# Kernel optimization log

Hardware: AMD Instinct MI355X
Metric: run time of the kernel (lower is better)

Reference implementation:

```python
import jax, jax.numpy as jnp
import numpy as np

BN_EPS = 1e-5


def _gcn(x, A, W, gamma, beta):
    # x: [B,N,Cin], A: [B,N,N] -> [B,N,Cout]; BatchNorm1d over (B,N) per channel (train-mode batch stats)
    h = jnp.einsum('bnm,bmc->bnc', A, x @ W)
    mu = h.mean(axis=(0, 1))
    var = h.var(axis=(0, 1))
    h = (h - mu) * jax.lax.rsqrt(var + BN_EPS) * gamma + beta
    return jax.nn.relu(h)  # dropout is identity (drop_prob=0 / eval)


def _ppige(x, A, W0, g0, b0, W_res, g_res, b_res):
    h = _gcn(x, A, W0, g0, b0)
    for i in range(W_res.shape[0]):  # residual GCN stack (num_GCN-1 layers)
        h = _gcn(h, A, W_res[i], g_res[i], b_res[i]) + h
    return h


def _gge(x, w1, b1, w2, b2):
    return jax.nn.relu(jax.nn.relu(x @ w1 + b1) @ w2 + b2)


def _gaga(G, h):
    # G: [B,N,H], h: [B,H]
    att = jax.nn.softmax(jnp.einsum('bnh,bh->bn', G, h), axis=-1)
    return jnp.einsum('bnh,bn->bh', G, att)


def _led(ea, eb, conv_w, conv_b, p1_w, p1_b, p2_w, p2_b):
    # ea, eb: [B, 2H]; Conv1d(2H->2H, k=1) over length-2 axis then MaxPool1d(2)
    stacked = jnp.stack([ea, eb], axis=-1)  # [B, 2H, 2]
    conv = jnp.einsum('oc,bct->bot', conv_w, stacked) + conv_b[None, :, None]
    cnn_x = conv.max(axis=-1)  # [B, 2H]
    x = jax.nn.relu(jnp.concatenate([cnn_x, ea - eb], axis=1) @ p1_w + p1_b)
    return x @ p2_w + p2_b


def setup_inputs() -> dict:
    key = jax.random.key(0)
    ks = jax.random.split(key, 24)
    Bs, N, PPI_in, H, F_in = 8, 2048, 512, 256, 1024
    n_res = 3  # num_GCN - 1
    s = 0.02
    adjA = jax.random.uniform(ks[0], (Bs, N, N), jnp.float32)
    adjB = jax.random.uniform(ks[1], (Bs, N, N), jnp.float32)
    adjA = adjA / adjA.sum(-1, keepdims=True)  # row-normalized for numerical sanity
    adjB = adjB / adjB.sum(-1, keepdims=True)
    return {
        'a': jax.random.normal(ks[2], (Bs, F_in), jnp.float32),
        'bio_a': jax.random.normal(ks[3], (Bs, N, PPI_in), jnp.float32),
        'A': adjA,
        'b': jax.random.normal(ks[4], (Bs, F_in), jnp.float32),
        'bio_b': jax.random.normal(ks[5], (Bs, N, PPI_in), jnp.float32),
        'B': adjB,
        'W0': jax.random.normal(ks[6], (PPI_in, H), jnp.float32) * s,
        'gamma0': jnp.ones((H,), jnp.float32),
        'beta0': jnp.zeros((H,), jnp.float32),
        'W_res': jax.random.normal(ks[7], (n_res, H, H), jnp.float32) * s,
        'gamma_res': jnp.ones((n_res, H), jnp.float32),
        'beta_res': jnp.zeros((n_res, H), jnp.float32),
        'g1_w': jax.random.normal(ks[8], (F_in, 128), jnp.float32) * s,
        'g1_b': jnp.zeros((128,), jnp.float32),
        'g2_w': jax.random.normal(ks[9], (128, H), jnp.float32) * s,
        'g2_b': jnp.zeros((H,), jnp.float32),
        'conv_w': jax.random.normal(ks[10], (2 * H, 2 * H), jnp.float32) * s,
        'conv_b': jnp.zeros((2 * H,), jnp.float32),
        'p1_w': jax.random.normal(ks[11], (4 * H, H), jnp.float32) * s,
        'p1_b': jnp.zeros((H,), jnp.float32),
        'p2_w': jax.random.normal(ks[12], (H, 2), jnp.float32) * s,
        'p2_b': jnp.zeros((2,), jnp.float32),
    }


def reference(a, bio_a, A, b, bio_b, B, W0, gamma0, beta0, W_res, gamma_res, beta_res,
              g1_w, g1_b, g2_w, g2_b, conv_w, conv_b, p1_w, p1_b, p2_w, p2_b):
    Ga = _ppige(bio_a, A, W0, gamma0, beta0, W_res, gamma_res, beta_res)
    Gb = _ppige(bio_b, B, W0, gamma0, beta0, W_res, gamma_res, beta_res)
    ha = _gge(a, g1_w, g1_b, g2_w, g2_b)
    hb = _gge(b, g1_w, g1_b, g2_w, g2_b)
    ea = jnp.concatenate([ha, _gaga(Ga, ha)], axis=-1)
    eb = jnp.concatenate([hb, _gaga(Gb, hb)], axis=-1)
    logits = _led(ea, eb, conv_w, conv_b, p1_w, p1_b, p2_w, p2_b)
    return jax.nn.log_softmax(logits, axis=-1)
```

## Files before the change

kernel.cpp:

```cpp
#include <hip/hip_runtime.h>
#include <hip/hip_bf16.h>
#include <cstdint>

typedef unsigned short u16;
typedef __bf16 bf16x8 __attribute__((ext_vector_type(8)));
typedef float f32x4 __attribute__((ext_vector_type(4)));

typedef __attribute__((address_space(1))) const void* gas_ptr;
typedef __attribute__((address_space(3))) void* las_ptr;

__device__ __forceinline__ u16 f2bf(float f) {
  union { __hip_bfloat16 h; u16 u; } v;
  v.h = __float2bfloat16(f);
  return v.u;
}
__device__ __forceinline__ float bf2f(u16 u) {
  union { unsigned int i; float f; } v;
  v.i = ((unsigned int)u) << 16;
  return v.f;
}

__device__ __forceinline__ void gload16(const u16* g, u16* l) {
  __builtin_amdgcn_global_load_lds((gas_ptr)g, (las_ptr)l, 16, 0, 0);
}

__global__ __launch_bounds__(256) void k_convert_all(const float* __restrict__ aA,
                                                     const float* __restrict__ aB,
                                                     const float* __restrict__ bA,
                                                     const float* __restrict__ bB,
                                                     u16* __restrict__ Abf,
                                                     u16* __restrict__ biobf) {
  long e0 = ((long)blockIdx.x * 256 + threadIdx.x) * 16;
  const float* src; u16* dst;
  if (e0 < 33554432L)        { src = aA;              dst = Abf; }
  else if (e0 < 67108864L)   { src = aB - 33554432L;  dst = Abf; }
  else if (e0 < 75497472L)   { src = bA - 67108864L;  dst = biobf - 67108864L; }
  else                       { src = bB - 75497472L;  dst = biobf - 75497472L + 8388608L; }
  float4 v0 = *reinterpret_cast<const float4*>(src + e0);
  float4 v1 = *reinterpret_cast<const float4*>(src + e0 + 4);
  float4 v2 = *reinterpret_cast<const float4*>(src + e0 + 8);
  float4 v3 = *reinterpret_cast<const float4*>(src + e0 + 12);
  union { u16 u[8]; uint4 q; } o0, o1;
  o0.u[0] = f2bf(v0.x); o0.u[1] = f2bf(v0.y); o0.u[2] = f2bf(v0.z); o0.u[3] = f2bf(v0.w);
  o0.u[4] = f2bf(v1.x); o0.u[5] = f2bf(v1.y); o0.u[6] = f2bf(v1.z); o0.u[7] = f2bf(v1.w);
  o1.u[0] = f2bf(v2.x); o1.u[1] = f2bf(v2.y); o1.u[2] = f2bf(v2.z); o1.u[3] = f2bf(v2.w);
  o1.u[4] = f2bf(v3.x); o1.u[5] = f2bf(v3.y); o1.u[6] = f2bf(v3.z); o1.u[7] = f2bf(v3.w);
  *reinterpret_cast<uint4*>(dst + e0) = o0.q;
  *reinterpret_cast<uint4*>(dst + e0 + 8) = o1.q;
}

__global__ __launch_bounds__(256) void k_prep_weights(const float* __restrict__ W0,
                                                      const float* __restrict__ Wres,
                                                      u16* __restrict__ W0t,
                                                      u16* __restrict__ Wrt) {
  __shared__ float tile[32][33];
  int y = blockIdx.y;
  const float* src; u16* dst; int R, r0;
  if (y < 16) { src = W0; dst = W0t; R = 512; r0 = y * 32; }
  else {
    int i = (y - 16) >> 3;
    src = Wres + i * 65536; dst = Wrt + i * 65536; R = 256; r0 = ((y - 16) & 7) * 32;
  }
  const int C = 256;
  int c0 = blockIdx.x * 32;
  int tx = threadIdx.x & 31, ty = threadIdx.x >> 5;
#pragma unroll
  for (int i = 0; i < 4; ++i) {
    int r = ty + i * 8;
    tile[r][tx] = src[(long)(r0 + r) * C + c0 + tx];
  }
  __syncthreads();
#pragma unroll
  for (int i = 0; i < 4; ++i) {
    int c = ty + i * 8;
    dst[(long)(c0 + c) * R + r0 + tx] = f2bf(tile[tx][c]);
  }
}

template<int EPI, int SWZ>
__global__ __launch_bounds__(256) void k_gemm(const u16* __restrict__ A, int lda, long sA,
                                              const u16* __restrict__ Bt, int ldb, long sB,
                                              u16* __restrict__ C, int ldc, long sC,
                                              u16* __restrict__ PtOut, int ldpt,
                                              float* __restrict__ stats, int K) {
  __shared__ __align__(16) u16 smem[4][8192];
  __shared__ float cs[256];
  const int tid = threadIdx.x;
  const int lane = tid & 63;
  const int wid = tid >> 6;
  const int wm = wid >> 1, wn = wid & 1;

  int bx = blockIdx.x, by = blockIdx.y, bz = blockIdx.z;
  if (SWZ) {
    int lin = bx + 16 * by + 32 * bz;
    int swz = (lin & 7) * 64 + (lin >> 3);
    bx = swz & 15; by = (swz >> 4) & 1; bz = swz >> 5;
  }
  const long m0 = (long)bx * 128, n0 = (long)by * 128;
  const int z = bz;
  const u16* Ab = A + (long)z * sA;
  const u16* Btb = Bt + (long)z * sB;

  const int rsub = lane >> 3;
  const int swzcol = ((lane & 7) ^ rsub) * 8;
  const long a_row = m0 + wid * 32 + rsub;
  const long b_row = n0 + wid * 32 + rsub;

  if (EPI == 0) cs[tid] = 0.f;

  const f32x4 zero = {0.f, 0.f, 0.f, 0.f};
  f32x4 acc[4][4];
#pragma unroll
  for (int i = 0; i < 4; ++i)
#pragma unroll
    for (int j = 0; j < 4; ++j) acc[i][j] = zero;

  const int fr = lane & 15;
  const int kgrp = lane >> 4;
  const int swz_rd = lane & 7;
  const int nk = K >> 6;

  auto stage = [&](int buf, int k0) {
#pragma unroll
    for (int i = 0; i < 4; ++i)
      gload16(Ab + (a_row + i * 8) * lda + (k0 + swzcol), &smem[buf][(wid * 32 + i * 8) * 64]);
#pragma unroll
    for (int i = 0; i < 4; ++i)
      gload16(Btb + (b_row + i * 8) * ldb + (k0 + swzcol), &smem[2 + buf][(wid * 32 + i * 8) * 64]);
  };

  stage(0, 0);
  __syncthreads();
  for (int t = 0; t < nk; ++t) {
    int cur = t & 1;
    if (t + 1 < nk) stage(1 - cur, (t + 1) * 64);
    const u16* Asb = smem[cur];
    const u16* Bsb = smem[2 + cur];
#pragma unroll
    for (int ks = 0; ks < 2; ++ks) {
      bf16x8 af[4], bfv[4];
#pragma unroll
      for (int f = 0; f < 4; ++f) {
        int cA = (ks * 4 + kgrp) ^ swz_rd;
        af[f]  = *reinterpret_cast<const bf16x8*>(&Asb[(wm * 64 + f * 16 + fr) * 64 + cA * 8]);
        bfv[f] = *reinterpret_cast<const bf16x8*>(&Bsb[(wn * 64 + f * 16 + fr) * 64 + cA * 8]);
      }
#pragma unroll
      for (int mf = 0; mf < 4; ++mf)
#pragma unroll
        for (int nf = 0; nf < 4; ++nf)
          acc[mf][nf] = __builtin_amdgcn_mfma_f32_16x16x32_bf16(af[mf], bfv[nf], acc[mf][nf], 0, 0, 0);
    }
    __syncthreads();
  }

  if (EPI == 0) {
    u16* Cb = C + (long)z * sC;
    const int side = z >> 3;
#pragma unroll
    for (int mf = 0; mf < 4; ++mf) {
      long mrow = m0 + wm * 64 + mf * 16 + kgrp * 4;
#pragma unroll
      for (int nf = 0; nf < 4; ++nf) {
        long ncol = n0 + wn * 64 + nf * 16 + fr;
#pragma unroll
        for (int r = 0; r < 4; ++r)
          Cb[(mrow + r) * ldc + ncol] = f2bf(acc[mf][nf][r]);
      }
    }
#pragma unroll
    for (int nf = 0; nf < 4; ++nf) {
      int cl = wn * 64 + nf * 16 + fr;
      float s = 0.f, q = 0.f;
#pragma unroll
      for (int mf = 0; mf < 4; ++mf)
#pragma unroll
        for (int r = 0; r < 4; ++r) { float v = acc[mf][nf][r]; s += v; q += v * v; }
      atomicAdd(&cs[cl], s);
      atomicAdd(&cs[128 + cl], q);
    }
    __syncthreads();
    if (tid < 128) atomicAdd(&stats[side * 512 + n0 + tid], cs[tid]);
    else           atomicAdd(&stats[side * 512 + 256 + n0 + (tid - 128)], cs[tid]);
  } else {
    u16* Ts = &smem[0][0];
#pragma unroll
    for (int mf = 0; mf < 4; ++mf)
#pragma unroll
      for (int nf = 0; nf < 4; ++nf) {
        int nl = wn * 64 + nf * 16 + fr;
        int ml = wm * 64 + mf * 16 + kgrp * 4;
#pragma unroll
        for (int r = 0; r < 4; ++r)
          Ts[nl * 136 + ml + r] = f2bf(acc[mf][nf][r]);
      }
    __syncthreads();
    int n = tid >> 1, half = tid & 1;
    const u16* sp = Ts + n * 136 + half * 64;
    u16* dp = PtOut + (long)(n0 + n) * ldpt + m0 + half * 64;
#pragma unroll
    for (int j = 0; j < 8; ++j)
      reinterpret_cast<uint4*>(dp)[j] = reinterpret_cast<const uint4*>(sp)[j];
  }
}

__global__ __launch_bounds__(256) void k_bn_apply(const ushort4* __restrict__ u4,
                                                  ushort4* __restrict__ h4,
                                                  const float* __restrict__ statsL,
                                                  const float* __restrict__ gamma,
                                                  const float* __restrict__ beta, int res) {
  long i = (long)blockIdx.x * 256 + threadIdx.x;
  int side = (int)(i >> 20);
  int c0 = (int)(i & 63) * 4;
  const float* st = statsL + side * 512;
  ushort4 uv = u4[i];
  float vp[4] = { bf2f(uv.x), bf2f(uv.y), bf2f(uv.z), bf2f(uv.w) };
  float rp[4];
#pragma unroll
  for (int j = 0; j < 4; ++j) {
    int c = c0 + j;
    float mu = st[c] * (1.f / 16384.f);
    float var = st[256 + c] * (1.f / 16384.f) - mu * mu;
    float sc = gamma[c] * rsqrtf(var + 1e-5f);
    float sh = beta[c] - mu * sc;
    rp[j] = fmaxf(vp[j] * sc + sh, 0.f);
  }
  if (res) {
    ushort4 hv = h4[i];
    rp[0] += bf2f(hv.x); rp[1] += bf2f(hv.y); rp[2] += bf2f(hv.z); rp[3] += bf2f(hv.w);
  }
  ushort4 o;
  o.x = f2bf(rp[0]); o.y = f2bf(rp[1]); o.z = f2bf(rp[2]); o.w = f2bf(rp[3]);
  h4[i] = o;
}

__global__ __launch_bounds__(256) void k_gge(const float* __restrict__ in_a,
                                             const float* __restrict__ in_b,
                                             const float* __restrict__ w1, const float* __restrict__ b1,
                                             const float* __restrict__ w2, const float* __restrict__ b2,
                                             float* __restrict__ ha) {
  __shared__ float av[1024];
  __shared__ float hid[128];
  int bx = blockIdx.x, t = threadIdx.x;
  const float* ap = ((bx >> 3) ? in_b : in_a) + (bx & 7) * 1024;
  for (int i = t; i < 1024; i += 256) av[i] = ap[i];
  __syncthreads();
  if (t < 128) {
    float s = b1[t];
    for (int c = 0; c < 1024; ++c) s += av[c] * w1[c * 128 + t];
    hid[t] = fmaxf(s, 0.f);
  }
  __syncthreads();
  float s = b2[t];
  for (int c = 0; c < 128; ++c) s += hid[c] * w2[c * 256 + t];
  ha[bx * 256 + t] = fmaxf(s, 0.f);
}

__global__ __launch_bounds__(256) void k_gaga_scores(const u16* __restrict__ h,
                                                     const float* __restrict__ ha,
                                                     float* __restrict__ sc) {
  __shared__ __align__(16) float has[256];
  int bx = blockIdx.x;
  has[threadIdx.x] = ha[bx * 256 + threadIdx.x];
  __syncthreads();
  const u16* G = h + (long)bx * 524288;
  int wv = threadIdx.x >> 6, lane = threadIdx.x & 63;
  float4 h4 = reinterpret_cast<const float4*>(has)[lane];
  for (int i = 0; i < 32; ++i) {
    int n = blockIdx.y * 128 + wv * 32 + i;
    ushort4 v = reinterpret_cast<const ushort4*>(G + (long)n * 256)[lane];
    float d = bf2f(v.x) * h4.x + bf2f(v.y) * h4.y + bf2f(v.z) * h4.z + bf2f(v.w) * h4.w;
#pragma unroll
    for (int o2 = 32; o2 > 0; o2 >>= 1) d += __shfl_down(d, o2);
    if (lane == 0) sc[bx * 2048 + n] = d;
  }
}

__global__ __launch_bounds__(256) void k_softmax2048(const float* __restrict__ sc, float* __restrict__ att) {
  __shared__ float red[256];
  int b = blockIdx.x, t = threadIdx.x;
  const float* s = sc + b * 2048;
  float* o = att + b * 2048;
  float v[8];
  float m = -1e30f;
#pragma unroll
  for (int i = 0; i < 8; ++i) { v[i] = s[t + i * 256]; m = fmaxf(m, v[i]); }
  red[t] = m; __syncthreads();
  for (int o2 = 128; o2 > 0; o2 >>= 1) { if (t < o2) red[t] = fmaxf(red[t], red[t + o2]); __syncthreads(); }
  m = red[0]; __syncthreads();
  float sum = 0.f;
#pragma unroll
  for (int i = 0; i < 8; ++i) { v[i] = expf(v[i] - m); sum += v[i]; }
  red[t] = sum; __syncthreads();
  for (int o2 = 128; o2 > 0; o2 >>= 1) { if (t < o2) red[t] += red[t + o2]; __syncthreads(); }
  float inv = 1.f / red[0];
#pragma unroll
  for (int i = 0; i < 8; ++i) o[t + i * 256] = v[i] * inv;
}

__global__ __launch_bounds__(256) void k_gaga_out(const u16* __restrict__ h,
                                                  const float* __restrict__ att,
                                                  float* __restrict__ ga) {
  __shared__ float atts[128];
  int bx = blockIdx.x, n0 = blockIdx.y * 128, c = threadIdx.x;
  if (threadIdx.x < 128) atts[threadIdx.x] = att[bx * 2048 + n0 + threadIdx.x];
  __syncthreads();
  const u16* base = h + (long)bx * 524288 + (long)n0 * 256 + c;
  float s = 0.f;
#pragma unroll 4
  for (int i = 0; i < 128; ++i) s += bf2f(base[(long)i * 256]) * atts[i];
  atomicAdd(&ga[bx * 256 + c], s);
}

__global__ __launch_bounds__(512) void k_led_conv(const float* __restrict__ ha, const float* __restrict__ ga,
                                                  const float* __restrict__ hb, const float* __restrict__ gb,
                                                  const float* __restrict__ cw, const float* __restrict__ cb,
                                                  float* __restrict__ cnn, float* __restrict__ diff) {
  __shared__ float ea[8][512], eb[8][512];
  int t = threadIdx.x;
  for (int i = t; i < 4096; i += 512) {
    int b = i >> 9, c = i & 511;
    float va = (c < 256) ? ha[b * 256 + c] : ga[b * 256 + c - 256];
    float vb = (c < 256) ? hb[b * 256 + c] : gb[b * 256 + c - 256];
    ea[b][c] = va; eb[b][c] = vb;
    if (blockIdx.x == 0) diff[i] = va - vb;
  }
  __syncthreads();
  int o = blockIdx.x * 64 + (t >> 3), b = t & 7;
  const float* wr = cw + (long)o * 512;
  float s0 = cb[o], s1 = s0;
  for (int c = 0; c < 512; ++c) { float w = wr[c]; s0 += w * ea[b][c]; s1 += w * eb[b][c]; }
  cnn[b * 512 + o] = fmaxf(s0, s1);
}

__global__ __launch_bounds__(256) void k_led_p1(const float* __restrict__ cnn, const float* __restrict__ diff,
                                                const float* __restrict__ w, const float* __restrict__ pb,
                                                float* __restrict__ x) {
  __shared__ float cat[8][1024];
  int t = threadIdx.x;
  for (int i = t; i < 8192; i += 256) {
    int b = i >> 10, c = i & 1023;
    cat[b][c] = (c < 512) ? cnn[b * 512 + c] : diff[b * 512 + c - 512];
  }
  __syncthreads();
  int o = blockIdx.x * 32 + (t >> 3), b = t & 7;
  float s = pb[o];
  for (int c = 0; c < 1024; ++c) s += cat[b][c] * w[c * 256 + o];
  x[b * 256 + o] = fmaxf(s, 0.f);
}

__global__ __launch_bounds__(64) void k_led_final(const float* __restrict__ x,
                                                  const float* __restrict__ p2w, const float* __restrict__ p2b,
                                                  float* __restrict__ out) {
  __shared__ float lg[16];
  int t = threadIdx.x;
  if (t < 16) {
    int b = t >> 1, j = t & 1;
    float s = p2b[j];
    for (int c = 0; c < 256; ++c) s += x[b * 256 + c] * p2w[c * 2 + j];
    lg[t] = s;
  }
  __syncthreads();
  if (t < 8) {
    float l0 = lg[t * 2], l1 = lg[t * 2 + 1];
    float m = fmaxf(l0, l1);
    float lse = m + logf(expf(l0 - m) + expf(l1 - m));
    out[t * 2] = l0 - lse;
    out[t * 2 + 1] = l1 - lse;
  }
}

extern "C" void kernel_launch(void* const* d_in, const int* in_sizes, int n_in,
                              void* d_out, int out_size, void* d_ws, size_t ws_size,
                              hipStream_t stream) {
  const float* in_a   = (const float*)d_in[0];
  const float* bio_a  = (const float*)d_in[1];
  const float* adj_a  = (const float*)d_in[2];
  const float* in_b   = (const float*)d_in[3];
  const float* bio_b  = (const float*)d_in[4];
  const float* adj_b  = (const float*)d_in[5];
  const float* W0     = (const float*)d_in[6];
  const float* gamma0 = (const float*)d_in[7];
  const float* beta0  = (const float*)d_in[8];
  const float* W_res  = (const float*)d_in[9];
  const float* g_res  = (const float*)d_in[10];
  const float* b_res  = (const float*)d_in[11];
  const float* g1_w   = (const float*)d_in[12];
  const float* g1_b   = (const float*)d_in[13];
  const float* g2_w   = (const float*)d_in[14];
  const float* g2_b   = (const float*)d_in[15];
  const float* conv_w = (const float*)d_in[16];
  const float* conv_b = (const float*)d_in[17];
  const float* p1_w   = (const float*)d_in[18];
  const float* p1_b   = (const float*)d_in[19];
  const float* p2_w   = (const float*)d_in[20];
  const float* p2_b   = (const float*)d_in[21];
  float* out = (float*)d_out;

  char* ws = (char*)d_ws;
  size_t off = 0;
  auto alloc = [&](size_t bytes) {
    char* p = ws + off;
    off += (bytes + 255) & ~(size_t)255;
    return p;
  };
  u16*   Abf   = (u16*)  alloc(67108864ull * 2);
  u16*   biobf = (u16*)  alloc(16777216ull * 2);
  u16*   Pt    = (u16*)  alloc(8388608ull * 2);
  u16*   ubf   = (u16*)  alloc(8388608ull * 2);
  u16*   hbf   = (u16*)  alloc(8388608ull * 2);
  u16*   W0t   = (u16*)  alloc(131072ull * 2);
  u16*   Wrt   = (u16*)  alloc(196608ull * 2);
  float* stats = (float*)alloc(4096 * 4);
  float* gabuf = (float*)alloc(4096 * 4);
  float* hav   = (float*)alloc(4096 * 4);
  float* scb   = (float*)alloc(32768 * 4);
  float* attb  = (float*)alloc(32768 * 4);
  float* cnn   = (float*)alloc(4096 * 4);
  float* diff  = (float*)alloc(4096 * 4);
  float* xbuf  = (float*)alloc(2048 * 4);

  k_prep_weights<<<dim3(8, 40), 256, 0, stream>>>(W0, W_res, W0t, Wrt);
  (void)hipMemsetAsync(stats, 0, 32768, stream);

  k_convert_all<<<20480, 256, 0, stream>>>(adj_a, adj_b, bio_a, bio_b, Abf, biobf);

  for (int layer = 0; layer < 4; ++layer) {
    const u16* Ain = (layer == 0) ? biobf : hbf;
    int K = (layer == 0) ? 512 : 256;
    const u16* Wt = (layer == 0) ? W0t : (Wrt + (layer - 1) * 65536);
    float* statsL = stats + layer * 1024;
    const float* gm = (layer == 0) ? gamma0 : (g_res + (layer - 1) * 256);
    const float* bt = (layer == 0) ? beta0 : (b_res + (layer - 1) * 256);

    k_gemm<1, 0><<<dim3(256, 2, 1), 256, 0, stream>>>(Ain, K, 0, Wt, K, 0,
                                                      nullptr, 0, 0, Pt, 32768, nullptr, K);
    k_gemm<0, 1><<<dim3(16, 2, 16), 256, 0, stream>>>(Abf, 2048, 4194304L, Pt, 32768, 2048,
                                                      ubf, 256, 524288L, nullptr, 0, statsL, 2048);
    k_bn_apply<<<8192, 256, 0, stream>>>((const ushort4*)ubf, (ushort4*)hbf,
                                         statsL, gm, bt, layer ? 1 : 0);
  }

  k_gge<<<16, 256, 0, stream>>>(in_a, in_b, g1_w, g1_b, g2_w, g2_b, hav);
  k_gaga_scores<<<dim3(16, 16), 256, 0, stream>>>(hbf, hav, scb);
  k_softmax2048<<<16, 256, 0, stream>>>(scb, attb);
  k_gaga_out<<<dim3(16, 16), 256, 0, stream>>>(hbf, attb, gabuf);

  k_led_conv<<<8, 512, 0, stream>>>(hav, gabuf, hav + 2048, gabuf + 2048, conv_w, conv_b, cnn, diff);
  k_led_p1<<<8, 256, 0, stream>>>(cnn, diff, p1_w, p1_b, xbuf);
  k_led_final<<<1, 64, 0, stream>>>(xbuf, p2_w, p2_b, out);
}
```

Baseline: 555.1 us.

## Fuse fp32-to-bf16 conversion into first-layer GEMMs and drop standalone convert pass

```diff
diff --git a/kernel.cpp b/kernel.cpp
--- a/kernel.cpp
+++ b/kernel.cpp
@@ -22,31 +22,6 @@
 
 __device__ __forceinline__ void gload16(const u16* g, u16* l) {
   __builtin_amdgcn_global_load_lds((gas_ptr)g, (las_ptr)l, 16, 0, 0);
-}
-
-__global__ __launch_bounds__(256) void k_convert_all(const float* __restrict__ aA,
-                                                     const float* __restrict__ aB,
-                                                     const float* __restrict__ bA,
-                                                     const float* __restrict__ bB,
-                                                     u16* __restrict__ Abf,
-                                                     u16* __restrict__ biobf) {
-  long e0 = ((long)blockIdx.x * 256 + threadIdx.x) * 16;
-  const float* src; u16* dst;
-  if (e0 < 33554432L)        { src = aA;              dst = Abf; }
-  else if (e0 < 67108864L)   { src = aB - 33554432L;  dst = Abf; }
-  else if (e0 < 75497472L)   { src = bA - 67108864L;  dst = biobf - 67108864L; }
-  else                       { src = bB - 75497472L;  dst = biobf - 75497472L + 8388608L; }
-  float4 v0 = *reinterpret_cast<const float4*>(src + e0);
-  float4 v1 = *reinterpret_cast<const float4*>(src + e0 + 4);
-  float4 v2 = *reinterpret_cast<const float4*>(src + e0 + 8);
-  float4 v3 = *reinterpret_cast<const float4*>(src + e0 + 12);
-  union { u16 u[8]; uint4 q; } o0, o1;
-  o0.u[0] = f2bf(v0.x); o0.u[1] = f2bf(v0.y); o0.u[2] = f2bf(v0.z); o0.u[3] = f2bf(v0.w);
-  o0.u[4] = f2bf(v1.x); o0.u[5] = f2bf(v1.y); o0.u[6] = f2bf(v1.z); o0.u[7] = f2bf(v1.w);
-  o1.u[0] = f2bf(v2.x); o1.u[1] = f2bf(v2.y); o1.u[2] = f2bf(v2.z); o1.u[3] = f2bf(v2.w);
-  o1.u[4] = f2bf(v3.x); o1.u[5] = f2bf(v3.y); o1.u[6] = f2bf(v3.z); o1.u[7] = f2bf(v3.w);
-  *reinterpret_cast<uint4*>(dst + e0) = o0.q;
-  *reinterpret_cast<uint4*>(dst + e0 + 8) = o1.q;
 }
 
 __global__ __launch_bounds__(256) void k_prep_weights(const float* __restrict__ W0,
@@ -77,12 +52,15 @@
   }
 }
 
-template<int EPI, int SWZ>
-__global__ __launch_bounds__(256) void k_gemm(const u16* __restrict__ A, int lda, long sA,
-                                              const u16* __restrict__ Bt, int ldb, long sB,
-                                              u16* __restrict__ C, int ldc, long sC,
-                                              u16* __restrict__ PtOut, int ldpt,
-                                              float* __restrict__ stats, int K) {
+template<int EPI, int SWZ, int CVT>
+__global__ __launch_bounds__(256) void k_gemm(
+    const u16* __restrict__ A, int lda, long sA,
+    const float* __restrict__ Afa, const float* __restrict__ Afb,
+    long splitRow, int ldaf, long zrows, u16* __restrict__ AbfOut,
+    const u16* __restrict__ Bt, int ldb, long sB,
+    u16* __restrict__ C, int ldc, long sC,
+    u16* __restrict__ PtOut, int ldpt,
+    float* __restrict__ stats, int K) {
   __shared__ __align__(16) u16 smem[4][8192];
   __shared__ float cs[256];
   const int tid = threadIdx.x;
@@ -91,10 +69,12 @@
   const int wm = wid >> 1, wn = wid & 1;
 
   int bx = blockIdx.x, by = blockIdx.y, bz = blockIdx.z;
-  if (SWZ) {
+  if (SWZ == 1) {
     int lin = bx + 16 * by + 32 * bz;
     int swz = (lin & 7) * 64 + (lin >> 3);
     bx = swz & 15; by = (swz >> 4) & 1; bz = swz >> 5;
+  } else if (SWZ == 2) {
+    int t = bx; bx = by; by = t;
   }
   const long m0 = (long)bx * 128, n0 = (long)by * 128;
   const int z = bz;
@@ -120,22 +100,17 @@
   const int swz_rd = lane & 7;
   const int nk = K >> 6;
 
-  auto stage = [&](int buf, int k0) {
+  auto stageA = [&](int buf, int k0) {
 #pragma unroll
     for (int i = 0; i < 4; ++i)
       gload16(Ab + (a_row + i * 8) * lda + (k0 + swzcol), &smem[buf][(wid * 32 + i * 8) * 64]);
+  };
+  auto stageB = [&](int buf, int k0) {
 #pragma unroll
     for (int i = 0; i < 4; ++i)
       gload16(Btb + (b_row + i * 8) * ldb + (k0 + swzcol), &smem[2 + buf][(wid * 32 + i * 8) * 64]);
   };
-
-  stage(0, 0);
-  __syncthreads();
-  for (int t = 0; t < nk; ++t) {
-    int cur = t & 1;
-    if (t + 1 < nk) stage(1 - cur, (t + 1) * 64);
-    const u16* Asb = smem[cur];
-    const u16* Bsb = smem[2 + cur];
+  auto compute = [&](const u16* Asb, const u16* Bsb) {
 #pragma unroll
     for (int ks = 0; ks < 2; ++ks) {
       bf16x8 af[4], bfv[4];
@@ -151,8 +126,61 @@
         for (int nf = 0; nf < 4; ++nf)
           acc[mf][nf] = __builtin_amdgcn_mfma_f32_16x16x32_bf16(af[mf], bfv[nf], acc[mf][nf], 0, 0, 0);
     }
+  };
+
+#define RLOADA(k0)                                                                       \
+  {                                                                                      \
+    _Pragma("unroll")                                                                    \
+    for (int i = 0; i < 4; ++i) {                                                        \
+      long R = (long)z * zrows + a_row + i * 8;                                          \
+      const float* sp = (R < splitRow ? Afa + R * (long)ldaf                             \
+                                      : Afb + (R - splitRow) * (long)ldaf) + (k0) + swzcol; \
+      rg[i * 2]     = *reinterpret_cast<const float4*>(sp);                              \
+      rg[i * 2 + 1] = *reinterpret_cast<const float4*>(sp + 4);                          \
+    }                                                                                    \
+  }
+#define CVTWRITEA(buf, k0)                                                               \
+  {                                                                                      \
+    _Pragma("unroll")                                                                    \
+    for (int i = 0; i < 4; ++i) {                                                        \
+      union { u16 u[8]; uint4 q; } o;                                                    \
+      o.u[0] = f2bf(rg[i*2].x);   o.u[1] = f2bf(rg[i*2].y);                              \
+      o.u[2] = f2bf(rg[i*2].z);   o.u[3] = f2bf(rg[i*2].w);                              \
+      o.u[4] = f2bf(rg[i*2+1].x); o.u[5] = f2bf(rg[i*2+1].y);                            \
+      o.u[6] = f2bf(rg[i*2+1].z); o.u[7] = f2bf(rg[i*2+1].w);                            \
+      *reinterpret_cast<uint4*>(&smem[buf][(wid * 32 + i * 8) * 64 + lane * 8]) = o.q;   \
+      if (AbfOut && by == 0) {                                                           \
+        long R = (long)z * zrows + a_row + i * 8;                                        \
+        *reinterpret_cast<uint4*>(AbfOut + R * (long)ldaf + (k0) + swzcol) = o.q;        \
+      }                                                                                  \
+    }                                                                                    \
+  }
+
+  if constexpr (CVT) {
+    float4 rg[8];
+    RLOADA(0);
+    stageB(0, 0);
+    CVTWRITEA(0, 0);
     __syncthreads();
-  }
+    for (int t = 0; t < nk; ++t) {
+      int cur = t & 1;
+      if (t + 1 < nk) { RLOADA((t + 1) * 64); stageB(1 - cur, (t + 1) * 64); }
+      compute(smem[cur], smem[2 + cur]);
+      if (t + 1 < nk) CVTWRITEA(1 - cur, (t + 1) * 64);
+      __syncthreads();
+    }
+  } else {
+    stageA(0, 0); stageB(0, 0);
+    __syncthreads();
+    for (int t = 0; t < nk; ++t) {
+      int cur = t & 1;
+      if (t + 1 < nk) { stageA(1 - cur, (t + 1) * 64); stageB(1 - cur, (t + 1) * 64); }
+      compute(smem[cur], smem[2 + cur]);
+      __syncthreads();
+    }
+  }
+#undef RLOADA
+#undef CVTWRITEA
 
   if (EPI == 0) {
     u16* Cb = C + (long)z * sC;
@@ -405,7 +433,6 @@
     return p;
   };
   u16*   Abf   = (u16*)  alloc(67108864ull * 2);
-  u16*   biobf = (u16*)  alloc(16777216ull * 2);
   u16*   Pt    = (u16*)  alloc(8388608ull * 2);
   u16*   ubf   = (u16*)  alloc(8388608ull * 2);
   u16*   hbf   = (u16*)  alloc(8388608ull * 2);
@@ -423,20 +450,27 @@
   k_prep_weights<<<dim3(8, 40), 256, 0, stream>>>(W0, W_res, W0t, Wrt);
   (void)hipMemsetAsync(stats, 0, 32768, stream);
 
-  k_convert_all<<<20480, 256, 0, stream>>>(adj_a, adj_b, bio_a, bio_b, Abf, biobf);
-
   for (int layer = 0; layer < 4; ++layer) {
-    const u16* Ain = (layer == 0) ? biobf : hbf;
-    int K = (layer == 0) ? 512 : 256;
-    const u16* Wt = (layer == 0) ? W0t : (Wrt + (layer - 1) * 65536);
     float* statsL = stats + layer * 1024;
     const float* gm = (layer == 0) ? gamma0 : (g_res + (layer - 1) * 256);
     const float* bt = (layer == 0) ? beta0 : (b_res + (layer - 1) * 256);
 
-    k_gemm<1, 0><<<dim3(256, 2, 1), 256, 0, stream>>>(Ain, K, 0, Wt, K, 0,
-                                                      nullptr, 0, 0, Pt, 32768, nullptr, K);
-    k_gemm<0, 1><<<dim3(16, 2, 16), 256, 0, stream>>>(Abf, 2048, 4194304L, Pt, 32768, 2048,
-                                                      ubf, 256, 524288L, nullptr, 0, statsL, 2048);
+    if (layer == 0) {
+      k_gemm<1, 2, 1><<<dim3(2, 256, 1), 256, 0, stream>>>(
+          nullptr, 0, 0, bio_a, bio_b, 16384L, 512, 0, nullptr,
+          W0t, 512, 0, nullptr, 0, 0, Pt, 32768, nullptr, 512);
+      k_gemm<0, 1, 1><<<dim3(16, 2, 16), 256, 0, stream>>>(
+          nullptr, 0, 0, adj_a, adj_b, 16384L, 2048, 2048, Abf,
+          Pt, 32768, 2048, ubf, 256, 524288L, nullptr, 0, statsL, 2048);
+    } else {
+      const u16* Wt = Wrt + (layer - 1) * 65536;
+      k_gemm<1, 2, 0><<<dim3(2, 256, 1), 256, 0, stream>>>(
+          hbf, 256, 0, nullptr, nullptr, 0, 0, 0, nullptr,
+          Wt, 256, 0, nullptr, 0, 0, Pt, 32768, nullptr, 256);
+      k_gemm<0, 1, 0><<<dim3(16, 2, 16), 256, 0, stream>>>(
+          Abf, 2048, 4194304L, nullptr, nullptr, 0, 0, 0, nullptr,
+          Pt, 32768, 2048, ubf, 256, 524288L, nullptr, 0, statsL, 2048);
+    }
     k_bn_apply<<<8192, 256, 0, stream>>>((const ushort4*)ubf, (ushort4*)hbf,
                                          statsL, gm, bt, layer ? 1 : 0);
   }
```

Measured after the change: 557.1 us. No clear change (+0.4%).
